# Kernel tuning notes

Hardware: AMD Instinct MI355X
Metric: run time of the kernel (lower is better)

Reference implementation:

```python
import jax, jax.numpy as jnp
import numpy as np

T = 3              # num_ntype (slots)
NH = 64            # num_hidden == num_classes
HEADS = (4, 4, 1)
NUM_ETYPES = 5
EDGE_DIM = 64
N_NODES = 20000
NEG_SLOPE = 0.2
ALPHA = 0.05       # residual-attention blend
EPS = 1e-12


def _l2_by_slot(x):
    # l2_norm with l2BySlot='True': normalize each ntype slot independently
    n = x.shape[0]
    xs = x.reshape(n, T, -1)
    nrm = jnp.linalg.norm(xs, axis=2, keepdims=True)
    return (xs / jnp.maximum(nrm, EPS)).reshape(n, -1)


def _edge_softmax(logits, dst, n):
    # softmax over incoming edges of each destination node
    m = jax.lax.stop_gradient(jax.ops.segment_max(logits, dst, num_segments=n))
    e = jnp.exp(logits - m[dst])
    s = jax.ops.segment_sum(e, dst, num_segments=n)
    return e / s[dst]


def _conv(x, src, dst, etype, W, al, ar, ee_tab, We, ae, res_attn, act):
    # slotGATConv: x [N,T,C], W [T,C,H*O], al/ar [H,T*O], ee_tab [R,De], We [De,H*De], ae [H,De]
    n = x.shape[0]
    H = al.shape[0]
    proj = jnp.einsum('ntc,tcd->ntd', x, W)                     # [N,T,H*O]
    O = proj.shape[-1] // H
    feat = proj.reshape(n, T, H, O).transpose(0, 2, 1, 3).reshape(n, H, T * O)
    el = jnp.einsum('nhd,hd->nh', feat, al)
    er = jnp.einsum('nhd,hd->nh', feat, ar)
    De = ee_tab.shape[1]
    ep = (ee_tab[etype] @ We).reshape(-1, H, De)                # [E,H,De]
    ee = jnp.einsum('ehd,hd->eh', ep, ae)                       # [E,H]
    logit = jax.nn.leaky_relu(el[src] + er[dst] + ee, NEG_SLOPE)
    a = _edge_softmax(logit, dst, n)                            # [E,H]
    if res_attn is not None:
        a = a * (1.0 - ALPHA) + res_attn * ALPHA
    out = jax.ops.segment_sum(feat[src] * a[:, :, None], dst, num_segments=n)  # [N,H,T*O]
    if act:
        out = jax.nn.elu(out)
    return out, a


def _forward(feat0, feat1, feat2, w_in0, b_in0, w_in1, b_in1, w_in2, b_in2,
             l0_W, l0_al, l0_ar, l0_ee, l0_we, l0_ae,
             l1_W, l1_al, l1_ar, l1_ee, l1_we, l1_ae,
             l2_W, l2_al, l2_ar, l2_ee, l2_we, l2_ae,
             dm_W, e_feat, src, dst, left, right, mid):
    feats = [feat0, feat1, feat2]
    lins = [(w_in0, b_in0), (w_in1, b_in1), (w_in2, b_in2)]
    blocks = []
    for t, (f, (w, b)) in enumerate(zip(feats, lins)):
        ft = f @ w + b                                          # [n_t, NH]
        pad = jnp.zeros((f.shape[0], T * NH), ft.dtype)
        blocks.append(pad.at[:, t * NH:(t + 1) * NH].set(ft))   # slot zero-padding
    h = jnp.concatenate(blocks, 0)                              # [N, T*NH]
    emb = [_l2_by_slot(h)]                                      # aggregator='None' -> identity
    x = h.reshape(-1, T, NH)
    out0, a0 = _conv(x, src, dst, e_feat, l0_W, l0_al, l0_ar, l0_ee, l0_we, l0_ae, None, True)
    emb.append(_l2_by_slot(out0.mean(1)))
    x = out0.reshape(-1, HEADS[0], T, NH).transpose(0, 2, 1, 3).reshape(-1, T, HEADS[0] * NH)
    out1, a1 = _conv(x, src, dst, e_feat, l1_W, l1_al, l1_ar, l1_ee, l1_we, l1_ae, a0, True)
    emb.append(_l2_by_slot(out1.mean(1)))
    x = out1.reshape(-1, HEADS[1], T, NH).transpose(0, 2, 1, 3).reshape(-1, T, HEADS[1] * NH)
    out2, _ = _conv(x, src, dst, e_feat, l2_W, l2_al, l2_ar, l2_ee, l2_we, l2_ae, a1, False)
    emb.append(_l2_by_slot(out2.mean(1)))
    # aggregator='None' + inProcessEmb='True': concat per-slot along feature dim
    embs = [e.reshape(-1, T, NH) for e in emb]
    o = jnp.concatenate(embs, 2).reshape(-1, T * NH * len(embs))  # [N, 768]
    le, re = o[left], o[right]
    scores = jnp.zeros(left.shape[0], o.dtype)
    for r in range(NUM_ETYPES):                                 # DistMult per relation
        s = ((le @ dm_W[r]) * re).sum(1)
        scores = jnp.where(mid == r, s, scores)
    return jax.nn.sigmoid(scores)


def setup_inputs() -> dict:
    key = jax.random.key(0)
    ks = iter(jax.random.split(key, 64))
    def nrm(shape, std):
        return jax.random.normal(next(ks), shape, jnp.float32) * std
    counts = [8000, 6000, 6000]
    in_dims = [256, 128, 64]
    inp = {}
    for t in range(T):
        inp[f'feat{t}'] = jax.random.normal(next(ks), (counts[t], in_dims[t]), jnp.float32)
        inp[f'w_in{t}'] = nrm((in_dims[t], NH), 0.1)
        inp[f'b_in{t}'] = nrm((NH,), 0.1)
    Cs = [NH, HEADS[0] * NH, HEADS[1] * NH]
    for l in range(3):
        H = HEADS[l]
        inp[f'l{l}_W'] = nrm((T, Cs[l], H * NH), 0.1)
        inp[f'l{l}_al'] = nrm((H, T * NH), 0.1)
        inp[f'l{l}_ar'] = nrm((H, T * NH), 0.1)
        inp[f'l{l}_ee'] = nrm((NUM_ETYPES, EDGE_DIM), 0.1)
        inp[f'l{l}_we'] = nrm((EDGE_DIM, H * EDGE_DIM), 0.1)
        inp[f'l{l}_ae'] = nrm((H, EDGE_DIM), 0.1)
    D = T * NH * 4
    inp['dm_W'] = nrm((NUM_ETYPES, D, D), 0.05)
    E, L = 200000, 10000
    inp['e_feat'] = jax.random.randint(next(ks), (E,), 0, NUM_ETYPES)
    inp['src'] = jax.random.randint(next(ks), (E,), 0, N_NODES)
    inp['dst'] = jax.random.randint(next(ks), (E,), 0, N_NODES)
    inp['left'] = jax.random.randint(next(ks), (L,), 0, N_NODES)
    inp['right'] = jax.random.randint(next(ks), (L,), 0, N_NODES)
    inp['mid'] = jax.random.randint(next(ks), (L,), 0, NUM_ETYPES)
    return inp


def reference(feat0, feat1, feat2, w_in0, b_in0, w_in1, b_in1, w_in2, b_in2,
              l0_W, l0_al, l0_ar, l0_ee, l0_we, l0_ae,
              l1_W, l1_al, l1_ar, l1_ee, l1_we, l1_ae,
              l2_W, l2_al, l2_ar, l2_ee, l2_we, l2_ae,
              dm_W, e_feat, src, dst, left, right, mid):
    return _forward(feat0, feat1, feat2, w_in0, b_in0, w_in1, b_in1, w_in2, b_in2,
                    l0_W, l0_al, l0_ar, l0_ee, l0_we, l0_ae,
                    l1_W, l1_al, l1_ar, l1_ee, l1_we, l1_ae,
                    l2_W, l2_al, l2_ar, l2_ee, l2_we, l2_ae,
                    dm_W, e_feat, src, dst, left, right, mid)
```

## Files before the change

### kernel.cpp

```cpp
#include <hip/hip_runtime.h>
#include <math.h>

#define N_NODES 20000
#define NPAD    20096
#define N_EDGES 200000
#define N_PAIRS 10000
#define PAIR_PAD 10368
#define DM_TILES 162
#define NBLK    79

typedef __attribute__((ext_vector_type(8))) short s16x8;
typedef __attribute__((ext_vector_type(4))) float f32x4;

__device__ inline float wave_max(float v){
  for (int o = 32; o > 0; o >>= 1) v = fmaxf(v, __shfl_xor(v, o));
  return v;
}
__device__ inline float wave_sum(float v){
  for (int o = 32; o > 0; o >>= 1) v += __shfl_xor(v, o);
  return v;
}
__device__ inline short f2bf(float x){
  union { float f; unsigned u; } v; v.f = x;
  unsigned r = (v.u + 0x7FFFu + ((v.u >> 16) & 1u)) >> 16;
  return (short)r;
}
__device__ inline float bf2f(short s){
  union { unsigned u; float f; } v; v.u = ((unsigned)(unsigned short)s) << 16;
  return v.f;
}

__global__ void build_h(const float* __restrict__ f0, const float* __restrict__ w0, const float* __restrict__ b0,
                        const float* __restrict__ f1, const float* __restrict__ w1, const float* __restrict__ b1,
                        const float* __restrict__ f2, const float* __restrict__ w2, const float* __restrict__ b2,
                        short* __restrict__ Xb0, short* __restrict__ o_b,
                        int* __restrict__ csr_cnt, int* __restrict__ cnt5, int* __restrict__ pos5,
                        float* __restrict__ score, int* __restrict__ pairs,
                        float* __restrict__ eall, short* __restrict__ Xb12){
  int n = blockIdx.x, lane = threadIdx.x;
  int idx64 = n * 64 + lane;
  if (lane == 0) csr_cnt[n] = 0;
  if (n == 0 && lane < 5){ cnt5[lane * 16] = 0; pos5[lane * 16] = 0; }
  if (idx64 < N_PAIRS + 16 && idx64 < 10016) score[idx64] = 0.f;
  if (idx64 < PAIR_PAD) pairs[idx64] = -1;
  if (idx64 < 480000) eall[idx64] = 0.f;
  s16x8 z = {};
  if (idx64 < 4608){
    int t = (idx64 * 16) / 24576, off = (idx64 * 16) % 24576;
    short* p = Xb12 + ((size_t)(t * NPAD + N_NODES)) * 256 + off;
    *(s16x8*)p = z; *(s16x8*)(p + 8) = z;
  }
  if (idx64 < 1152){
    int t = (idx64 * 16) / 6144, off = (idx64 * 16) % 6144;
    short* p = Xb0 + ((size_t)(t * NPAD + N_NODES)) * 64 + off;
    *(s16x8*)p = z; *(s16x8*)(p + 8) = z;
  }
  int t, idx, C; const float *f, *w, *b;
  if (n < 8000)       { t = 0; idx = n;         C = 256; f = f0; w = w0; b = b0; }
  else if (n < 14000) { t = 1; idx = n - 8000;  C = 128; f = f1; w = w1; b = b1; }
  else                { t = 2; idx = n - 14000; C = 64;  f = f2; w = w2; b = b2; }
  __shared__ float xs[256];
  for (int c = lane; c < C; c += 64) xs[c] = f[(size_t)idx * C + c];
  __syncthreads();
  float acc = b[lane];
  for (int c = 0; c < C; c++) acc += xs[c] * w[c * 64 + lane];
  for (int tt = 0; tt < 3; tt++)
    Xb0[((size_t)(tt * NPAD) + n) * 64 + lane] = f2bf((tt == t) ? acc : 0.f);
  float ss = wave_sum(acc * acc);
  float sc = 1.f / fmaxf(sqrtf(ss), 1e-12f);
  for (int tt = 0; tt < 3; tt++)
    o_b[(size_t)n * 768 + tt * 256 + lane] = f2bf((tt == t) ? acc * sc : 0.f);
}

__global__ void count_k(const int* __restrict__ dst, int* __restrict__ csr_cnt,
                        const int* __restrict__ mid, int* __restrict__ cnt5){
  int e = blockIdx.x * 256 + threadIdx.x;
  int lane = threadIdx.x & 63;
  if (e < N_EDGES) atomicAdd(&csr_cnt[dst[e]], 1);
  int r_mine = (e < N_PAIRS) ? mid[e] : -1;
#pragma unroll
  for (int r = 0; r < 5; r++){
    unsigned long long mask = __ballot(r_mine == r);
    if (mask){
      int leader = __ffsll((long long)mask) - 1;
      if (lane == leader) atomicAdd(&cnt5[r * 16], __popcll(mask));
    }
  }
}

__global__ void scan1_k(const int* __restrict__ cnt, int* __restrict__ loc, int* __restrict__ bsum){
  __shared__ int s[256];
  int tid = threadIdx.x;
  int idx = blockIdx.x * 256 + tid;
  int v = (idx < N_NODES) ? cnt[idx] : 0;
  s[tid] = v;
  __syncthreads();
  for (int o = 1; o < 256; o <<= 1){
    int u = (tid >= o) ? s[tid - o] : 0;
    __syncthreads();
    s[tid] += u;
    __syncthreads();
  }
  if (idx < N_NODES) loc[idx] = s[tid] - v;
  if (tid == 255) bsum[blockIdx.x] = s[255];
}

__global__ void scan2_k(const int* __restrict__ bsum, int* __restrict__ bofs,
                        const int* __restrict__ cnt5, int* __restrict__ off5){
  __shared__ int s[128];
  int tid = threadIdx.x;
  int v = (tid < NBLK) ? bsum[tid] : 0;
  s[tid] = v;
  __syncthreads();
  for (int o = 1; o < 128; o <<= 1){
    int u = (tid >= o) ? s[tid - o] : 0;
    __syncthreads();
    s[tid] += u;
    __syncthreads();
  }
  if (tid < NBLK) bofs[tid] = s[tid] - v;
  if (tid == 0){
    int r0 = 0;
    for (int r = 0; r < 5; r++){ off5[r] = r0; r0 += ((cnt5[r * 16] + 63) >> 6) << 6; }
  }
}

__global__ void scan3_k(const int* __restrict__ loc, const int* __restrict__ bofs,
                        int* __restrict__ coff, int* __restrict__ cpos){
  int idx = blockIdx.x * 256 + threadIdx.x;
  if (idx < N_NODES){
    int v = loc[idx] + bofs[blockIdx.x];
    coff[idx] = v;
    cpos[idx * 16] = v;
  }
  if (idx == 0) coff[N_NODES] = N_EDGES;
}

__global__ void scatter_k(const int* __restrict__ dst, const int* __restrict__ srcv,
                          const int* __restrict__ efeat, int* __restrict__ cpos,
                          int* __restrict__ src_sorted, int* __restrict__ et_sorted,
                          const int* __restrict__ mid, const int* __restrict__ off5,
                          int* __restrict__ pos5, int* __restrict__ pairs){
  int e = blockIdx.x * 256 + threadIdx.x;
  int lane = threadIdx.x & 63;
  if (e < N_EDGES){
    int p = atomicAdd(&cpos[dst[e] * 16], 1);
    src_sorted[p] = srcv[e];
    et_sorted[p] = efeat[e];
  }
  int r_mine = (e < N_PAIRS) ? mid[e] : -1;
#pragma unroll
  for (int r = 0; r < 5; r++){
    unsigned long long mask = __ballot(r_mine == r);
    if (mask){
      int cnt = __popcll(mask);
      int leader = __ffsll((long long)mask) - 1;
      int base = 0;
      if (lane == leader) base = atomicAdd(&pos5[r * 16], cnt);
      base = __shfl(base, leader);
      if (r_mine == r){
        int rank = __popcll(mask & ((1ull << lane) - 1ull));
        pairs[off5[r] + base + rank] = e;
      }
    }
  }
}

__global__ void prep_k(const float* __restrict__ lW0, const float* __restrict__ lW1,
                       const float* __restrict__ lW2, const float* __restrict__ dmW,
                       short* __restrict__ Wt0, short* __restrict__ Wt1,
                       short* __restrict__ Wt2, short* __restrict__ Mt,
                       const float* __restrict__ ee0, const float* __restrict__ we0, const float* __restrict__ ae0,
                       const float* __restrict__ ee1, const float* __restrict__ we1, const float* __restrict__ ae1,
                       const float* __restrict__ ee2, const float* __restrict__ we2, const float* __restrict__ ae2,
                       float* __restrict__ ee5f){
  const int bx = blockIdx.x, by = blockIdx.y, z = blockIdx.z;
  if (z == 10){
    int r = bx, L = by;
    if (r >= 5 || L >= 3) return;
    int H = (L == 2) ? 1 : 4;
    const float* eetab = (L == 0) ? ee0 : ((L == 1) ? ee1 : ee2);
    const float* We    = (L == 0) ? we0 : ((L == 1) ? we1 : we2);
    const float* ae    = (L == 0) ? ae0 : ((L == 1) ? ae1 : ae2);
    int h = threadIdx.x >> 6, lane = threadIdx.x & 63;
    if (h >= H) return;
    float v = 0.f;
    for (int k = 0; k < 64; k++) v += eetab[r * 64 + k] * We[k * H * 64 + h * 64 + lane];
    v *= ae[h * 64 + lane];
    v = wave_sum(v);
    if (lane == 0) ee5f[L * 32 + r * H + h] = v;
    return;
  }
  const float* s; short* d; int R, Cc, r0, c0;
  if (z < 5){
    s = dmW + (size_t)z * 589824; d = Mt + (size_t)z * 589824;
    R = 768; Cc = 768; r0 = bx * 32; c0 = by * 32;
  } else if (z < 8){
    if (bx >= 8 || by >= 8) return;
    int t = z - 5;
    s = lW1 + (size_t)t * 65536; d = Wt1 + (size_t)t * 65536;
    R = 256; Cc = 256; r0 = bx * 32; c0 = by * 32;
  } else if (z == 8){
    if (bx >= 6 || by >= 8) return;
    int t = bx >> 1;
    s = lW0 + (size_t)t * 16384; d = Wt0 + (size_t)t * 16384;
    R = 64; Cc = 256; r0 = (bx & 1) * 32; c0 = by * 32;
  } else {
    if (bx >= 8 || by >= 6) return;
    int t = by >> 1;
    s = lW2 + (size_t)t * 16384; d = Wt2 + (size_t)t * 16384;
    R = 256; Cc = 64; r0 = bx * 32; c0 = (by & 1) * 32;
  }
  __shared__ float tile[32][33];
  int tx = threadIdx.x & 31, ty = threadIdx.x >> 5;
  for (int i = 0; i < 32; i += 8){
    int r = r0 + ty + i;
    tile[ty + i][tx] = (r < R && c0 + tx < Cc) ? s[(size_t)r * Cc + c0 + tx] : 0.f;
  }
  __syncthreads();
  for (int i = 0; i < 32; i += 8){
    int c = c0 + ty + i;
    if (c < Cc && r0 + tx < R)
      d[(size_t)c * R + r0 + tx] = f2bf(tile[tx][ty + i]);
  }
}

template<int C, int NO>
__global__ void mfma_proj(const short* __restrict__ Xb, const short* __restrict__ Wt,
                          short* __restrict__ featb, const float* __restrict__ al,
                          const float* __restrict__ ar, float* __restrict__ elf,
                          float* __restrict__ erf){
  constexpr int H = NO / 64;
  const int n0 = blockIdx.x * 128;
  const int ct = blockIdx.y;
  const int t  = blockIdx.z;
  const int tid = threadIdx.x;
  const int w = tid >> 6, lane = tid & 63;
  const int quad = lane >> 4, ln = lane & 15;
  __shared__ __attribute__((aligned(16))) short A_s[128 * 32];
  __shared__ __attribute__((aligned(16))) short B_s[64 * 32];
  const short* Xt  = Xb + (size_t)t * NPAD * C;
  const short* Wtt = Wt + ((size_t)t * NO + ct * 64) * C;
  f32x4 acc[2][4] = {};
  for (int kk = 0; kk < C; kk += 32){
    {
      int row = tid >> 1, half = tid & 1;
      const s16x8* g = (const s16x8*)(Xt + (size_t)(n0 + row) * C + kk + half * 16);
      s16x8 v0 = g[0], v1 = g[1];
      *(s16x8*)(A_s + row * 32 + half * 16) = v0;
      *(s16x8*)(A_s + row * 32 + half * 16 + 8) = v1;
    }
    {
      int row = tid >> 2, chunk = tid & 3;
      s16x8 v = *(const s16x8*)(Wtt + (size_t)row * C + kk + chunk * 8);
      *(s16x8*)(B_s + row * 32 + chunk * 8) = v;
    }
    __syncthreads();
    s16x8 af0 = *(s16x8*)(A_s + (w * 32 + ln) * 32 + quad * 8);
    s16x8 af1 = *(s16x8*)(A_s + (w * 32 + 16 + ln) * 32 + quad * 8);
    s16x8 bf[4];
#pragma unroll
    for (int b = 0; b < 4; b++) bf[b] = *(s16x8*)(B_s + (b * 16 + ln) * 32 + quad * 8);
#pragma unroll
    for (int b = 0; b < 4; b++){
      acc[0][b] = __builtin_amdgcn_mfma_f32_16x16x32_bf16(af0, bf[b], acc[0][b], 0, 0, 0);
      acc[1][b] = __builtin_amdgcn_mfma_f32_16x16x32_bf16(af1, bf[b], acc[1][b], 0, 0, 0);
    }
    __syncthreads();
  }
#pragma unroll
  for (int ar_ = 0; ar_ < 2; ar_++){
#pragma unroll
    for (int i = 0; i < 4; i++){
      int n = n0 + w * 32 + ar_ * 16 + quad * 4 + i;
      if (n >= N_NODES) continue;
#pragma unroll
      for (int b = 0; b < 4; b++){
        int jj = b * 16 + ln;
        featb[((size_t)n * H + ct) * 192 + t * 64 + jj] = f2bf(acc[ar_][b][i]);
      }
    }
  }
  float alv[4], arv[4];
#pragma unroll
  for (int b = 0; b < 4; b++){
    alv[b] = al[ct * 192 + t * 64 + b * 16 + ln];
    arv[b] = ar[ct * 192 + t * 64 + b * 16 + ln];
  }
#pragma unroll
  for (int ar_ = 0; ar_ < 2; ar_++){
#pragma unroll
    for (int i = 0; i < 4; i++){
      float pe = 0.f, pr = 0.f;
#pragma unroll
      for (int b = 0; b < 4; b++){
        pe += acc[ar_][b][i] * alv[b];
        pr += acc[ar_][b][i] * arv[b];
      }
#pragma unroll
      for (int o = 1; o < 16; o <<= 1){
        pe += __shfl_xor(pe, o);
        pr += __shfl_xor(pr, o);
      }
      int n = n0 + w * 32 + ar_ * 16 + quad * 4 + i;
      if (ln == 0 && n < N_NODES){
        atomicAdd(&elf[n * H + ct], pe);
        atomicAdd(&erf[n * H + ct], pr);
      }
    }
  }
}

template<int H, int MODE, int ACT>
__global__ __launch_bounds__(256) void gat_fused(
    const int* __restrict__ csr_off, const int* __restrict__ src_sorted,
    const int* __restrict__ et_sorted,
    const float* __restrict__ el, const float* __restrict__ er, const float* __restrict__ ee5,
    const float* __restrict__ aprev, float* __restrict__ aout,
    const short* __restrict__ featb, short* __restrict__ outb,
    short* __restrict__ o_b, int kslice){
  const int wid = threadIdx.x >> 6, lane = threadIdx.x & 63;
  const int n = blockIdx.x * 4 + wid;
  if (n >= N_NODES) return;
  constexpr int NC = H * 192 / 8;
  const int c0 = lane, h0 = (c0 / 24) % H;
  const int c1 = lane + 64, h1 = (c1 / 24) % H;
  const bool act0 = (c0 < NC);
  const bool act1 = (H == 4) && (lane < 32);
  const int off = csr_off[n];
  const int cnt = csr_off[n + 1] - off;
  __shared__ float a_s[4][64][H];
  __shared__ float out_s[4][H * 192];
  float acc0[8] = {}, acc1[8] = {};
  float ern[H];
#pragma unroll
  for (int h = 0; h < H; h++) ern[h] = er[n * H + h];

  if (cnt > 0 && cnt <= 64){
    int p = off + lane;
    int sidx = 0, r = 0;
    if (lane < cnt){ sidx = src_sorted[p]; r = et_sorted[p]; }
    float lg[H];
#pragma unroll
    for (int h = 0; h < H; h++) lg[h] = -1e30f;
    if (lane < cnt){
#pragma unroll
      for (int h = 0; h < H; h++){
        float v = el[sidx * H + h] + ern[h] + ee5[r * H + h];
        lg[h] = (v >= 0.f) ? v : 0.2f * v;
      }
    }
    float ap[4] = {};
    if (MODE > 0 && lane < cnt){
#pragma unroll
      for (int q = 0; q < 4; q++) ap[q] = aprev[(size_t)p * 4 + q];
    }
    float av[H];
#pragma unroll
    for (int h = 0; h < H; h++){
      float mh = wave_max(lg[h]);
      float ex = (lane < cnt) ? __expf(lg[h] - mh) : 0.f;
      float sh = wave_sum(ex);
      float a = ex / sh;
      if (MODE == 1) a = 0.95f * a + 0.05f * ap[h];
      if (MODE == 2) a = 0.95f * a + 0.0125f * (ap[0] + ap[1] + ap[2] + ap[3]);
      av[h] = a;
      if (lane < cnt) a_s[wid][lane][h] = a;
    }
    if (MODE != 2 && lane < cnt){
      f32x4 o = {av[0], av[1], av[2], av[3]};
      *(f32x4*)(aout + (size_t)p * 4) = o;
    }
    int b = 0;
    for (; b + 4 <= cnt; b += 4){
      int p4 = off + b;
      int s0 = src_sorted[p4],     s1 = src_sorted[p4 + 1];
      int s2 = src_sorted[p4 + 2], s3 = src_sorted[p4 + 3];
      s16x8 v00, v01, v02, v03, v10, v11, v12, v13;
      if (act0){
        v00 = *(const s16x8*)(featb + (size_t)s0 * (H * 192) + c0 * 8);
        v01 = *(const s16x8*)(featb + (size_t)s1 * (H * 192) + c0 * 8);
        v02 = *(const s16x8*)(featb + (size_t)s2 * (H * 192) + c0 * 8);
        v03 = *(const s16x8*)(featb + (size_t)s3 * (H * 192) + c0 * 8);
      }
      if (act1){
        v10 = *(const s16x8*)(featb + (size_t)s0 * (H * 192) + c1 * 8);
        v11 = *(const s16x8*)(featb + (size_t)s1 * (H * 192) + c1 * 8);
        v12 = *(const s16x8*)(featb + (size_t)s2 * (H * 192) + c1 * 8);
        v13 = *(const s16x8*)(featb + (size_t)s3 * (H * 192) + c1 * 8);
      }
      if (act0){
        float a0 = a_s[wid][b][h0], a1 = a_s[wid][b + 1][h0];
        float a2 = a_s[wid][b + 2][h0], a3 = a_s[wid][b + 3][h0];
#pragma unroll
        for (int i = 0; i < 8; i++)
          acc0[i] += a0 * bf2f(v00[i]) + a1 * bf2f(v01[i]) +
                     a2 * bf2f(v02[i]) + a3 * bf2f(v03[i]);
      }
      if (act1){
        float a0 = a_s[wid][b][h1], a1 = a_s[wid][b + 1][h1];
        float a2 = a_s[wid][b + 2][h1], a3 = a_s[wid][b + 3][h1];
#pragma unroll
        for (int i = 0; i < 8; i++)
          acc1[i] += a0 * bf2f(v10[i]) + a1 * bf2f(v11[i]) +
                     a2 * bf2f(v12[i]) + a3 * bf2f(v13[i]);
      }
    }
    for (; b < cnt; b++){
      int pp = off + b;
      int s = src_sorted[pp];
      if (act0){
        float a = a_s[wid][b][h0];
        s16x8 v = *(const s16x8*)(featb + (size_t)s * (H * 192) + c0 * 8);
#pragma unroll
        for (int i = 0; i < 8; i++) acc0[i] += a * bf2f(v[i]);
      }
      if (act1){
        float a = a_s[wid][b][h1];
        s16x8 v = *(const s16x8*)(featb + (size_t)s * (H * 192) + c1 * 8);
#pragma unroll
        for (int i = 0; i < 8; i++) acc1[i] += a * bf2f(v[i]);
      }
    }
  } else if (cnt > 64){
    float mh[H], sh[H];
#pragma unroll
    for (int h = 0; h < H; h++){ mh[h] = -1e30f; sh[h] = 0.f; }
    for (int b = lane; b < cnt; b += 64){
      int p = off + b; int s = src_sorted[p]; int r = et_sorted[p];
#pragma unroll
      for (int h = 0; h < H; h++){
        float v = el[s * H + h] + ern[h] + ee5[r * H + h];
        v = (v >= 0.f) ? v : 0.2f * v;
        mh[h] = fmaxf(mh[h], v);
      }
    }
#pragma unroll
    for (int h = 0; h < H; h++) mh[h] = wave_max(mh[h]);
    for (int b = lane; b < cnt; b += 64){
      int p = off + b; int s = src_sorted[p]; int r = et_sorted[p];
#pragma unroll
      for (int h = 0; h < H; h++){
        float v = el[s * H + h] + ern[h] + ee5[r * H + h];
        v = (v >= 0.f) ? v : 0.2f * v;
        sh[h] += __expf(v - mh[h]);
      }
    }
#pragma unroll
    for (int h = 0; h < H; h++) sh[h] = wave_sum(sh[h]);
    if (MODE != 2){
      for (int b = lane; b < cnt; b += 64){
        int p = off + b; int s = src_sorted[p]; int r = et_sorted[p];
        float ap[4] = {};
        if (MODE > 0){
#pragma unroll
          for (int q = 0; q < 4; q++) ap[q] = aprev[(size_t)p * 4 + q];
        }
        float av[4] = {};
#pragma unroll
        for (int h = 0; h < H; h++){
          float v = el[s * H + h] + ern[h] + ee5[r * H + h];
          v = (v >= 0.f) ? v : 0.2f * v;
          float a = __expf(v - mh[h]) / sh[h];
          if (MODE == 1) a = 0.95f * a + 0.05f * ap[h];
          av[h] = a;
        }
        f32x4 o = {av[0], av[1], av[2], av[3]};
        *(f32x4*)(aout + (size_t)p * 4) = o;
      }
    }
    for (int b = 0; b < cnt; b++){
      int p = off + b; int s = src_sorted[p]; int r = et_sorted[p];
      const short* row = featb + (size_t)s * (H * 192);
      float apm[4] = {};
      if (MODE > 0){
#pragma unroll
        for (int q = 0; q < 4; q++) apm[q] = aprev[(size_t)p * 4 + q];
      }
      if (act0){
        float v = el[s * H + h0] + ern[h0] + ee5[r * H + h0];
        v = (v >= 0.f) ? v : 0.2f * v;
        float a = __expf(v - mh[h0]) / sh[h0];
        if (MODE == 1) a = 0.95f * a + 0.05f * apm[h0];
        if (MODE == 2) a = 0.95f * a + 0.0125f * (apm[0] + apm[1] + apm[2] + apm[3]);
        s16x8 vv = *(const s16x8*)(row + c0 * 8);
#pragma unroll
        for (int i = 0; i < 8; i++) acc0[i] += a * bf2f(vv[i]);
      }
      if (act1){
        float v = el[s * H + h1] + ern[h1] + ee5[r * H + h1];
        v = (v >= 0.f) ? v : 0.2f * v;
        float a = __expf(v - mh[h1]) / sh[h1];
        if (MODE == 1) a = 0.95f * a + 0.05f * apm[h1];
        s16x8 vv = *(const s16x8*)(row + c1 * 8);
#pragma unroll
        for (int i = 0; i < 8; i++) acc1[i] += a * bf2f(vv[i]);
      }
    }
  }
  if (act0){
    int dd = c0 * 8, h = dd / 192, rr = dd % 192, t = rr / 64, j = rr % 64;
    if (ACT){
#pragma unroll
      for (int i = 0; i < 8; i++) acc0[i] = (acc0[i] > 0.f) ? acc0[i] : expm1f(acc0[i]);
    }
#pragma unroll
    for (int i = 0; i < 8; i++) out_s[wid][dd + i] = acc0[i];
    if (outb){
      s16x8 o;
#pragma unroll
      for (int i = 0; i < 8; i++) o[i] = f2bf(acc0[i]);
      *(s16x8*)(outb + ((size_t)(t * NPAD) + n) * 256 + h * 64 + j) = o;
    }
  }
  if (act1){
    int dd = c1 * 8, h = dd / 192, rr = dd % 192, t = rr / 64, j = rr % 64;
    if (ACT){
#pragma unroll
      for (int i = 0; i < 8; i++) acc1[i] = (acc1[i] > 0.f) ? acc1[i] : expm1f(acc1[i]);
    }
#pragma unroll
    for (int i = 0; i < 8; i++) out_s[wid][dd + i] = acc1[i];
    if (outb){
      s16x8 o;
#pragma unroll
      for (int i = 0; i < 8; i++) o[i] = f2bf(acc1[i]);
      *(s16x8*)(outb + ((size_t)(t * NPAD) + n) * 256 + h * 64 + j) = o;
    }
  }
  for (int t = 0; t < 3; t++){
    float v;
    if (H == 4)
      v = 0.25f * (out_s[wid][t * 64 + lane] + out_s[wid][192 + t * 64 + lane] +
                   out_s[wid][384 + t * 64 + lane] + out_s[wid][576 + t * 64 + lane]);
    else
      v = out_s[wid][t * 64 + lane];
    float ss = wave_sum(v * v);
    float sc = 1.f / fmaxf(sqrtf(ss), 1e-12f);
    o_b[(size_t)n * 768 + t * 256 + kslice * 64 + lane] = f2bf(v * sc);
  }
}

__global__ void distmult_mfma(const short* __restrict__ o_b, const short* __restrict__ Mt,
                              const int* __restrict__ pairs, const int* __restrict__ left,
                              const int* __restrict__ right, const int* __restrict__ mid,
                              float* __restrict__ score){
  const int pt = blockIdx.x, ct = blockIdx.y;
  const int tid = threadIdx.x;
  const int w = tid >> 6, lane = tid & 63;
  const int quad = lane >> 4, ln = lane & 15;
  __shared__ __attribute__((aligned(16))) short smem[8192];
  short* A_s = smem;
  short* B_s = smem + 2048;
  __shared__ int pid_s[64];
  __shared__ int lbase[64];
  if (tid < 64){
    int p = pairs[pt * 64 + tid];
    pid_s[tid] = p;
    lbase[tid] = (p >= 0) ? left[p] * 768 : 0;
  }
  __syncthreads();
  int p0 = pid_s[0];
  if (p0 < 0) return;
  const int r = mid[p0];
  const short* Mr = Mt + (size_t)r * 768 * 768;
  f32x4 acc[8] = {};
  for (int kk = 0; kk < 768; kk += 32){
    {
      int row = tid >> 2, chunk = tid & 3;
      s16x8 v = *(const s16x8*)(o_b + (size_t)lbase[row] + kk + chunk * 8);
      *(s16x8*)(A_s + row * 32 + chunk * 8) = v;
    }
    {
      int row = tid >> 1, half = tid & 1;
      const s16x8* g = (const s16x8*)(Mr + (size_t)(ct * 128 + row) * 768 + kk + half * 16);
      s16x8 v0 = g[0], v1 = g[1];
      *(s16x8*)(B_s + row * 32 + half * 16) = v0;
      *(s16x8*)(B_s + row * 32 + half * 16 + 8) = v1;
    }
    __syncthreads();
    s16x8 af = *(s16x8*)(A_s + (w * 16 + ln) * 32 + quad * 8);
#pragma unroll
    for (int b = 0; b < 8; b++){
      s16x8 bf = *(s16x8*)(B_s + (b * 16 + ln) * 32 + quad * 8);
      acc[b] = __builtin_amdgcn_mfma_f32_16x16x32_bf16(af, bf, acc[b], 0, 0, 0);
    }
    __syncthreads();
  }
  short* RE_s = smem;
  {
    int row = tid >> 2, quarter = tid & 3;
    int p = pid_s[row];
    s16x8 v0 = {}, v1 = {}, v2 = {}, v3 = {};
    if (p >= 0){
      const s16x8* g = (const s16x8*)(o_b + (size_t)right[p] * 768 + ct * 128 + quarter * 32);
      v0 = g[0]; v1 = g[1]; v2 = g[2]; v3 = g[3];
    }
    __syncthreads();
    short* dst = RE_s + row * 128 + quarter * 32;
    *(s16x8*)(dst)      = v0;
    *(s16x8*)(dst + 8)  = v1;
    *(s16x8*)(dst + 16) = v2;
    *(s16x8*)(dst + 24) = v3;
  }
  __syncthreads();
#pragma unroll
  for (int i = 0; i < 4; i++){
    int row = w * 16 + quad * 4 + i;
    float s = 0.f;
#pragma unroll
    for (int b = 0; b < 8; b++)
      s += acc[b][i] * bf2f(RE_s[row * 128 + b * 16 + ln]);
    s += __shfl_xor(s, 1); s += __shfl_xor(s, 2);
    s += __shfl_xor(s, 4); s += __shfl_xor(s, 8);
    if (ln == 0){
      int p = pid_s[row];
      if (p >= 0) atomicAdd(&score[p], s);
    }
  }
}

__global__ void sigmoid_k(const float* __restrict__ score, float* __restrict__ out){
  int i = blockIdx.x * 256 + threadIdx.x;
  if (i < N_PAIRS) out[i] = 1.f / (1.f + __expf(-score[i]));
}

extern "C" void kernel_launch(void* const* d_in, const int* in_sizes, int n_in,
                              void* d_out, int out_size, void* d_ws, size_t ws_size,
                              hipStream_t stream){
  const float* f0 = (const float*)d_in[0];
  const float* w0 = (const float*)d_in[1];
  const float* b0 = (const float*)d_in[2];
  const float* f1 = (const float*)d_in[3];
  const float* w1 = (const float*)d_in[4];
  const float* b1 = (const float*)d_in[5];
  const float* f2 = (const float*)d_in[6];
  const float* w2_ = (const float*)d_in[7];
  const float* b2 = (const float*)d_in[8];
  const float* lW[3]  = {(const float*)d_in[9],  (const float*)d_in[15], (const float*)d_in[21]};
  const float* lal[3] = {(const float*)d_in[10], (const float*)d_in[16], (const float*)d_in[22]};
  const float* lar[3] = {(const float*)d_in[11], (const float*)d_in[17], (const float*)d_in[23]};
  const float* lee[3] = {(const float*)d_in[12], (const float*)d_in[18], (const float*)d_in[24]};
  const float* lwe[3] = {(const float*)d_in[13], (const float*)d_in[19], (const float*)d_in[25]};
  const float* lae[3] = {(const float*)d_in[14], (const float*)d_in[20], (const float*)d_in[26]};
  const float* dmW = (const float*)d_in[27];
  const int* efeat = (const int*)d_in[28];
  const int* srcv  = (const int*)d_in[29];
  const int* dstv  = (const int*)d_in[30];
  const int* left  = (const int*)d_in[31];
  const int* right = (const int*)d_in[32];
  const int* midv  = (const int*)d_in[33];
  float* out = (float*)d_out;

  short* feat_b = (short*)d_ws;
  float* aA     = (float*)(feat_b + 15360000);
  float* aB     = aA + 800000;
  float* eall   = aB + 800000;
  float* ee5f   = eall + 480000;
  float* score  = ee5f + 96;
  int* csr_cnt  = (int*)(score + 10016);
  int* csr_off  = csr_cnt + 20000;
  int* csr_pos  = csr_off + 20004;
  int* loc      = csr_pos + 320000;
  int* bsum     = loc + 20000;
  int* bofs     = bsum + 128;
  int* src_sorted = bofs + 128;
  int* et_sorted  = src_sorted + 200000;
  int* cnt5     = et_sorted + 200000;
  int* off5     = cnt5 + 80;
  int* pos5     = off5 + 8;
  int* pairs    = pos5 + 80;
  short* o_b    = (short*)(pairs + PAIR_PAD);
  short* Xb0    = o_b + 15360000;
  short* Xb12   = Xb0 + 3858432;
  short* Wt0    = Xb12 + 15433728;
  short* Wt1    = Wt0 + 49152;
  short* Wt2    = Wt1 + 196608;
  short* Mt     = Wt2 + 49152;
  float* elf0 = eall, *erf0 = eall + 80000;
  float* elf1 = eall + 160000, *erf1 = eall + 240000;
  float* elf2 = eall + 320000, *erf2 = eall + 400000;

  build_h<<<N_NODES, 64, 0, stream>>>(f0, w0, b0, f1, w1, b1, f2, w2_, b2, Xb0, o_b,
                                      csr_cnt, cnt5, pos5, score, pairs, eall, Xb12);
  count_k<<<782, 256, 0, stream>>>(dstv, csr_cnt, midv, cnt5);
  scan1_k<<<NBLK, 256, 0, stream>>>(csr_cnt, loc, bsum);
  scan2_k<<<1, 128, 0, stream>>>(bsum, bofs, cnt5, off5);
  scan3_k<<<NBLK, 256, 0, stream>>>(loc, bofs, csr_off, csr_pos);
  scatter_k<<<782, 256, 0, stream>>>(dstv, srcv, efeat, csr_pos, src_sorted, et_sorted,
                                     midv, off5, pos5, pairs);
  { dim3 g(24, 24, 11);
    prep_k<<<g, 256, 0, stream>>>(lW[0], lW[1], lW[2], dmW, Wt0, Wt1, Wt2, Mt,
                                  lee[0], lwe[0], lae[0], lee[1], lwe[1], lae[1],
                                  lee[2], lwe[2], lae[2], ee5f); }

  { dim3 g(NPAD / 128, 4, 3);
    mfma_proj<64, 256><<<g, 256, 0, stream>>>(Xb0, Wt0, feat_b, lal[0], lar[0], elf0, erf0); }
  gat_fused<4, 0, 1><<<5000, 256, 0, stream>>>(csr_off, src_sorted, et_sorted, elf0, erf0, ee5f,
                                               nullptr, aA, feat_b, Xb12, o_b, 1);

  { dim3 g(NPAD / 128, 4, 3);
    mfma_proj<256, 256><<<g, 256, 0, stream>>>(Xb12, Wt1, feat_b, lal[1], lar[1], elf1, erf1); }
  gat_fused<4, 1, 1><<<5000, 256, 0, stream>>>(csr_off, src_sorted, et_sorted, elf1, erf1, ee5f + 32,
                                               aA, aB, feat_b, Xb12, o_b, 2);

  { dim3 g(NPAD / 128, 1, 3);
    mfma_proj<256, 64><<<g, 256, 0, stream>>>(Xb12, Wt2, feat_b, lal[2], lar[2], elf2, erf2); }
  gat_fused<1, 2, 0><<<5000, 256, 0, stream>>>(csr_off, src_sorted, et_sorted, elf2, erf2, ee5f + 64,
                                               aB, nullptr, feat_b, nullptr, o_b, 3);

  { dim3 g(DM_TILES, 6); distmult_mfma<<<g, 256, 0, stream>>>(o_b, Mt, pairs, left, right, midv, score); }
  sigmoid_k<<<40, 256, 0, stream>>>(score, out);
}
```

Before: 530.9 us.

## Skip zero-slot tiles in layer-0 projection and merge count with prep kernel

Layer-0 inputs are nonzero only in their own node-type slot, so the first projection now runs only over the row tiles belonging to each type (62/48/48 of 157 tiles per slot). The zero-slot projected features are written as zeros directly in build_h. The edge-count kernel and the weight-prep kernel are fused into one launch, and the prep work moves ahead of the scans. This removes roughly two thirds of the layer-0 projection MFMA work and one launch. The cost is extra stores in build_h, and correctness depends on the hardcoded type ranges (0-8000, 8000-14000, 14000-20000) and the tile bounds, which overlap by one tile at each boundary.

```diff
diff --git a/kernel.cpp b/kernel.cpp
--- a/kernel.cpp
+++ b/kernel.cpp
@@ -36,12 +36,13 @@
                         short* __restrict__ Xb0, short* __restrict__ o_b,
                         int* __restrict__ csr_cnt, int* __restrict__ cnt5, int* __restrict__ pos5,
                         float* __restrict__ score, int* __restrict__ pairs,
-                        float* __restrict__ eall, short* __restrict__ Xb12){
+                        float* __restrict__ eall, short* __restrict__ Xb12,
+                        short* __restrict__ featb){
   int n = blockIdx.x, lane = threadIdx.x;
   int idx64 = n * 64 + lane;
   if (lane == 0) csr_cnt[n] = 0;
   if (n == 0 && lane < 5){ cnt5[lane * 16] = 0; pos5[lane * 16] = 0; }
-  if (idx64 < N_PAIRS + 16 && idx64 < 10016) score[idx64] = 0.f;
+  if (idx64 < 10016) score[idx64] = 0.f;
   if (idx64 < PAIR_PAD) pairs[idx64] = -1;
   if (idx64 < 480000) eall[idx64] = 0.f;
   s16x8 z = {};
@@ -59,6 +60,13 @@
   if (n < 8000)       { t = 0; idx = n;         C = 256; f = f0; w = w0; b = b0; }
   else if (n < 14000) { t = 1; idx = n - 8000;  C = 128; f = f1; w = w1; b = b1; }
   else                { t = 2; idx = n - 14000; C = 64;  f = f2; w = w2; b = b2; }
+  {
+    int h = lane >> 4, si = (lane >> 3) & 1, j8 = lane & 7;
+    int s0 = (t == 0) ? 1 : 0;
+    int s1 = (t == 2) ? 1 : 2;
+    int toff = si ? s1 : s0;
+    *(s16x8*)(featb + ((size_t)n * 4 + h) * 192 + toff * 64 + j8 * 8) = z;
+  }
   __shared__ float xs[256];
   for (int c = lane; c < C; c += 64) xs[c] = f[(size_t)idx * C + c];
   __syncthreads();
@@ -72,109 +80,35 @@
     o_b[(size_t)n * 768 + tt * 256 + lane] = f2bf((tt == t) ? acc * sc : 0.f);
 }
 
-__global__ void count_k(const int* __restrict__ dst, int* __restrict__ csr_cnt,
-                        const int* __restrict__ mid, int* __restrict__ cnt5){
-  int e = blockIdx.x * 256 + threadIdx.x;
-  int lane = threadIdx.x & 63;
-  if (e < N_EDGES) atomicAdd(&csr_cnt[dst[e]], 1);
-  int r_mine = (e < N_PAIRS) ? mid[e] : -1;
-#pragma unroll
-  for (int r = 0; r < 5; r++){
-    unsigned long long mask = __ballot(r_mine == r);
-    if (mask){
-      int leader = __ffsll((long long)mask) - 1;
-      if (lane == leader) atomicAdd(&cnt5[r * 16], __popcll(mask));
-    }
-  }
-}
-
-__global__ void scan1_k(const int* __restrict__ cnt, int* __restrict__ loc, int* __restrict__ bsum){
-  __shared__ int s[256];
-  int tid = threadIdx.x;
-  int idx = blockIdx.x * 256 + tid;
-  int v = (idx < N_NODES) ? cnt[idx] : 0;
-  s[tid] = v;
-  __syncthreads();
-  for (int o = 1; o < 256; o <<= 1){
-    int u = (tid >= o) ? s[tid - o] : 0;
-    __syncthreads();
-    s[tid] += u;
-    __syncthreads();
-  }
-  if (idx < N_NODES) loc[idx] = s[tid] - v;
-  if (tid == 255) bsum[blockIdx.x] = s[255];
-}
-
-__global__ void scan2_k(const int* __restrict__ bsum, int* __restrict__ bofs,
-                        const int* __restrict__ cnt5, int* __restrict__ off5){
-  __shared__ int s[128];
-  int tid = threadIdx.x;
-  int v = (tid < NBLK) ? bsum[tid] : 0;
-  s[tid] = v;
-  __syncthreads();
-  for (int o = 1; o < 128; o <<= 1){
-    int u = (tid >= o) ? s[tid - o] : 0;
-    __syncthreads();
-    s[tid] += u;
-    __syncthreads();
-  }
-  if (tid < NBLK) bofs[tid] = s[tid] - v;
-  if (tid == 0){
-    int r0 = 0;
-    for (int r = 0; r < 5; r++){ off5[r] = r0; r0 += ((cnt5[r * 16] + 63) >> 6) << 6; }
-  }
-}
-
-__global__ void scan3_k(const int* __restrict__ loc, const int* __restrict__ bofs,
-                        int* __restrict__ coff, int* __restrict__ cpos){
-  int idx = blockIdx.x * 256 + threadIdx.x;
-  if (idx < N_NODES){
-    int v = loc[idx] + bofs[blockIdx.x];
-    coff[idx] = v;
-    cpos[idx * 16] = v;
-  }
-  if (idx == 0) coff[N_NODES] = N_EDGES;
-}
-
-__global__ void scatter_k(const int* __restrict__ dst, const int* __restrict__ srcv,
-                          const int* __restrict__ efeat, int* __restrict__ cpos,
-                          int* __restrict__ src_sorted, int* __restrict__ et_sorted,
-                          const int* __restrict__ mid, const int* __restrict__ off5,
-                          int* __restrict__ pos5, int* __restrict__ pairs){
-  int e = blockIdx.x * 256 + threadIdx.x;
-  int lane = threadIdx.x & 63;
-  if (e < N_EDGES){
-    int p = atomicAdd(&cpos[dst[e] * 16], 1);
-    src_sorted[p] = srcv[e];
-    et_sorted[p] = efeat[e];
-  }
-  int r_mine = (e < N_PAIRS) ? mid[e] : -1;
-#pragma unroll
-  for (int r = 0; r < 5; r++){
-    unsigned long long mask = __ballot(r_mine == r);
-    if (mask){
-      int cnt = __popcll(mask);
-      int leader = __ffsll((long long)mask) - 1;
-      int base = 0;
-      if (lane == leader) base = atomicAdd(&pos5[r * 16], cnt);
-      base = __shfl(base, leader);
-      if (r_mine == r){
-        int rank = __popcll(mask & ((1ull << lane) - 1ull));
-        pairs[off5[r] + base + rank] = e;
-      }
-    }
-  }
-}
-
-__global__ void prep_k(const float* __restrict__ lW0, const float* __restrict__ lW1,
-                       const float* __restrict__ lW2, const float* __restrict__ dmW,
-                       short* __restrict__ Wt0, short* __restrict__ Wt1,
-                       short* __restrict__ Wt2, short* __restrict__ Mt,
-                       const float* __restrict__ ee0, const float* __restrict__ we0, const float* __restrict__ ae0,
-                       const float* __restrict__ ee1, const float* __restrict__ we1, const float* __restrict__ ae1,
-                       const float* __restrict__ ee2, const float* __restrict__ we2, const float* __restrict__ ae2,
-                       float* __restrict__ ee5f){
-  const int bx = blockIdx.x, by = blockIdx.y, z = blockIdx.z;
+__global__ void count_prep_k(const int* __restrict__ dst, int* __restrict__ csr_cnt,
+                             const int* __restrict__ mid, int* __restrict__ cnt5,
+                             const float* __restrict__ lW0, const float* __restrict__ lW1,
+                             const float* __restrict__ lW2, const float* __restrict__ dmW,
+                             short* __restrict__ Wt0, short* __restrict__ Wt1,
+                             short* __restrict__ Wt2, short* __restrict__ Mt,
+                             const float* __restrict__ ee0, const float* __restrict__ we0, const float* __restrict__ ae0,
+                             const float* __restrict__ ee1, const float* __restrict__ we1, const float* __restrict__ ae1,
+                             const float* __restrict__ ee2, const float* __restrict__ we2, const float* __restrict__ ae2,
+                             float* __restrict__ ee5f){
+  if (blockIdx.x < 782){
+    int e = blockIdx.x * 256 + threadIdx.x;
+    int lane = threadIdx.x & 63;
+    if (e < N_EDGES) atomicAdd(&csr_cnt[dst[e]], 1);
+    int r_mine = (e < N_PAIRS) ? mid[e] : -1;
+#pragma unroll
+    for (int r = 0; r < 5; r++){
+      unsigned long long mask = __ballot(r_mine == r);
+      if (mask){
+        int leader = __ffsll((long long)mask) - 1;
+        if (lane == leader) atomicAdd(&cnt5[r * 16], __popcll(mask));
+      }
+    }
+    return;
+  }
+  int lin = blockIdx.x - 782;
+  int z = lin / 576;
+  int rem = lin % 576;
+  int by = rem / 24, bx = rem % 24;
   if (z == 10){
     int r = bx, L = by;
     if (r >= 5 || L >= 3) return;
@@ -225,15 +159,100 @@
   }
 }
 
-template<int C, int NO>
+__global__ void scan1_k(const int* __restrict__ cnt, int* __restrict__ loc, int* __restrict__ bsum){
+  __shared__ int s[256];
+  int tid = threadIdx.x;
+  int idx = blockIdx.x * 256 + tid;
+  int v = (idx < N_NODES) ? cnt[idx] : 0;
+  s[tid] = v;
+  __syncthreads();
+  for (int o = 1; o < 256; o <<= 1){
+    int u = (tid >= o) ? s[tid - o] : 0;
+    __syncthreads();
+    s[tid] += u;
+    __syncthreads();
+  }
+  if (idx < N_NODES) loc[idx] = s[tid] - v;
+  if (tid == 255) bsum[blockIdx.x] = s[255];
+}
+
+__global__ void scan2_k(const int* __restrict__ bsum, int* __restrict__ bofs,
+                        const int* __restrict__ cnt5, int* __restrict__ off5){
+  __shared__ int s[128];
+  int tid = threadIdx.x;
+  int v = (tid < NBLK) ? bsum[tid] : 0;
+  s[tid] = v;
+  __syncthreads();
+  for (int o = 1; o < 128; o <<= 1){
+    int u = (tid >= o) ? s[tid - o] : 0;
+    __syncthreads();
+    s[tid] += u;
+    __syncthreads();
+  }
+  if (tid < NBLK) bofs[tid] = s[tid] - v;
+  if (tid == 0){
+    int r0 = 0;
+    for (int r = 0; r < 5; r++){ off5[r] = r0; r0 += ((cnt5[r * 16] + 63) >> 6) << 6; }
+  }
+}
+
+__global__ void scan3_k(const int* __restrict__ loc, const int* __restrict__ bofs,
+                        int* __restrict__ coff, int* __restrict__ cpos){
+  int idx = blockIdx.x * 256 + threadIdx.x;
+  if (idx < N_NODES){
+    int v = loc[idx] + bofs[blockIdx.x];
+    coff[idx] = v;
+    cpos[idx * 16] = v;
+  }
+  if (idx == 0) coff[N_NODES] = N_EDGES;
+}
+
+__global__ void scatter_k(const int* __restrict__ dst, const int* __restrict__ srcv,
+                          const int* __restrict__ efeat, int* __restrict__ cpos,
+                          int* __restrict__ src_sorted, int* __restrict__ et_sorted,
+                          const int* __restrict__ mid, const int* __restrict__ off5,
+                          int* __restrict__ pos5, int* __restrict__ pairs){
+  int e = blockIdx.x * 256 + threadIdx.x;
+  int lane = threadIdx.x & 63;
+  if (e < N_EDGES){
+    int p = atomicAdd(&cpos[dst[e] * 16], 1);
+    src_sorted[p] = srcv[e];
+    et_sorted[p] = efeat[e];
+  }
+  int r_mine = (e < N_PAIRS) ? mid[e] : -1;
+#pragma unroll
+  for (int r = 0; r < 5; r++){
+    unsigned long long mask = __ballot(r_mine == r);
+    if (mask){
+      int cnt = __popcll(mask);
+      int leader = __ffsll((long long)mask) - 1;
+      int base = 0;
+      if (lane == leader) base = atomicAdd(&pos5[r * 16], cnt);
+      base = __shfl(base, leader);
+      if (r_mine == r){
+        int rank = __popcll(mask & ((1ull << lane) - 1ull));
+        pairs[off5[r] + base + rank] = e;
+      }
+    }
+  }
+}
+
+template<int C, int NO, int TYPED>
 __global__ void mfma_proj(const short* __restrict__ Xb, const short* __restrict__ Wt,
                           short* __restrict__ featb, const float* __restrict__ al,
                           const float* __restrict__ ar, float* __restrict__ elf,
                           float* __restrict__ erf){
   constexpr int H = NO / 64;
-  const int n0 = blockIdx.x * 128;
   const int ct = blockIdx.y;
   const int t  = blockIdx.z;
+  int tile = blockIdx.x;
+  if (TYPED){
+    const int lo[3] = {0, 62, 109};
+    const int hi[3] = {63, 110, 157};
+    tile += lo[t];
+    if (tile >= hi[t]) return;
+  }
+  const int n0 = tile * 128;
   const int tid = threadIdx.x;
   const int w = tid >> 6, lane = tid & 63;
   const int quad = lane >> 4, ln = lane & 15;
@@ -682,30 +701,29 @@
   float* elf2 = eall + 320000, *erf2 = eall + 400000;
 
   build_h<<<N_NODES, 64, 0, stream>>>(f0, w0, b0, f1, w1, b1, f2, w2_, b2, Xb0, o_b,
-                                      csr_cnt, cnt5, pos5, score, pairs, eall, Xb12);
-  count_k<<<782, 256, 0, stream>>>(dstv, csr_cnt, midv, cnt5);
+                                      csr_cnt, cnt5, pos5, score, pairs, eall, Xb12, feat_b);
+  count_prep_k<<<782 + 6336, 256, 0, stream>>>(dstv, csr_cnt, midv, cnt5,
+                                               lW[0], lW[1], lW[2], dmW, Wt0, Wt1, Wt2, Mt,
+                                               lee[0], lwe[0], lae[0], lee[1], lwe[1], lae[1],
+                                               lee[2], lwe[2], lae[2], ee5f);
   scan1_k<<<NBLK, 256, 0, stream>>>(csr_cnt, loc, bsum);
   scan2_k<<<1, 128, 0, stream>>>(bsum, bofs, cnt5, off5);
   scan3_k<<<NBLK, 256, 0, stream>>>(loc, bofs, csr_off, csr_pos);
   scatter_k<<<782, 256, 0, stream>>>(dstv, srcv, efeat, csr_pos, src_sorted, et_sorted,
                                      midv, off5, pos5, pairs);
-  { dim3 g(24, 24, 11);
-    prep_k<<<g, 256, 0, stream>>>(lW[0], lW[1], lW[2], dmW, Wt0, Wt1, Wt2, Mt,
-                                  lee[0], lwe[0], lae[0], lee[1], lwe[1], lae[1],
-                                  lee[2], lwe[2], lae[2], ee5f); }
-
-  { dim3 g(NPAD / 128, 4, 3);
-    mfma_proj<64, 256><<<g, 256, 0, stream>>>(Xb0, Wt0, feat_b, lal[0], lar[0], elf0, erf0); }
+
+  { dim3 g(64, 4, 3);
+    mfma_proj<64, 256, 1><<<g, 256, 0, stream>>>(Xb0, Wt0, feat_b, lal[0], lar[0], elf0, erf0); }
   gat_fused<4, 0, 1><<<5000, 256, 0, stream>>>(csr_off, src_sorted, et_sorted, elf0, erf0, ee5f,
                                                nullptr, aA, feat_b, Xb12, o_b, 1);
 
   { dim3 g(NPAD / 128, 4, 3);
-    mfma_proj<256, 256><<<g, 256, 0, stream>>>(Xb12, Wt1, feat_b, lal[1], lar[1], elf1, erf1); }
+    mfma_proj<256, 256, 0><<<g, 256, 0, stream>>>(Xb12, Wt1, feat_b, lal[1], lar[1], elf1, erf1); }
   gat_fused<4, 1, 1><<<5000, 256, 0, stream>>>(csr_off, src_sorted, et_sorted, elf1, erf1, ee5f + 32,
                                                aA, aB, feat_b, Xb12, o_b, 2);
 
   { dim3 g(NPAD / 128, 1, 3);
-    mfma_proj<256, 64><<<g, 256, 0, stream>>>(Xb12, Wt2, feat_b, lal[2], lar[2], elf2, erf2); }
+    mfma_proj<256, 64, 0><<<g, 256, 0, stream>>>(Xb12, Wt2, feat_b, lal[2], lar[2], elf2, erf2); }
   gat_fused<1, 2, 0><<<5000, 256, 0, stream>>>(csr_off, src_sorted, et_sorted, elf2, erf2, ee5f + 64,
                                                aB, nullptr, feat_b, nullptr, o_b, 3);
 
```

Measured after the change: 503.5 us. -5.2%, faster.
